# Performance work log

Hardware: AMD Instinct MI355X
Metric: run time of the kernel (lower is better)

The kernel has to match this reference:

```python
import jax, jax.numpy as jnp
import numpy as np

B, S, D = 2, 2048, 1024
N_HEADS = 16
HEAD_DIM = D // N_HEADS  # 64, even for RoPE
THETA = 10000.0


def rope_tables(seq, head_dim, dtype=jnp.float32):
    half = head_dim // 2
    freqs = 1.0 / (THETA ** (jnp.arange(half, dtype=jnp.float32) / half))
    angles = jnp.arange(seq, dtype=jnp.float32)[:, None] * freqs[None, :]  # [S, half]
    return jnp.cos(angles).astype(dtype), jnp.sin(angles).astype(dtype)


def apply_rope_interleaved(x, cos, sin):
    # x: [b, h, s, d]; even/odd interleaving
    x_even = x[..., 0::2]
    x_odd = x[..., 1::2]
    r_even = x_even * cos - x_odd * sin
    r_odd = x_even * sin + x_odd * cos
    # interleave back: stack on last axis then reshape
    out = jnp.stack([r_even, r_odd], axis=-1).reshape(x.shape)
    return out


def setup_inputs() -> dict:
    key = jax.random.key(0)
    ks = jax.random.split(key, 6)
    scale = 1.0 / np.sqrt(D)
    return {
        "x": jax.random.normal(ks[0], (B, S, D), dtype=jnp.float32),
        "Wq": jax.random.normal(ks[1], (D, D), dtype=jnp.float32) * scale,
        "Wk": jax.random.normal(ks[2], (D, D), dtype=jnp.float32) * scale,
        "Wv": jax.random.normal(ks[3], (D, D), dtype=jnp.float32) * scale,
        "Wo": jax.random.normal(ks[4], (D, D), dtype=jnp.float32) * scale,
        "bo": jnp.zeros((D,), dtype=jnp.float32),
    }


def reference(x, Wq, Wk, Wv, Wo, bo):
    b, s, _ = x.shape
    # QKV projections (no bias), split heads -> [b, h, s, hd]
    def proj(W):
        return jnp.einsum('bsd,de->bse', x, W).reshape(b, s, N_HEADS, HEAD_DIM).transpose(0, 2, 1, 3)
    q, k, v = proj(Wq), proj(Wk), proj(Wv)

    cos, sin = rope_tables(s, HEAD_DIM, x.dtype)  # [s, hd//2]
    q = apply_rope_interleaved(q, cos, sin)
    k = apply_rope_interleaved(k, cos, sin)

    scale = 1.0 / jnp.sqrt(jnp.asarray(HEAD_DIM, dtype=x.dtype))
    scores = jnp.einsum('bhqd,bhkd->bhqk', q, k) * scale  # [b, h, s, s]
    causal = jnp.tril(jnp.ones((s, s), dtype=bool))
    scores = jnp.where(causal[None, None], scores, jnp.asarray(-jnp.inf, dtype=scores.dtype))
    attn = jax.nn.softmax(scores, axis=-1)
    ctx = jnp.einsum('bhqk,bhkd->bhqd', attn, v)  # [b, h, s, hd]
    ctx = ctx.transpose(0, 2, 1, 3).reshape(b, s, N_HEADS * HEAD_DIM)
    return jnp.einsum('bsd,de->bse', ctx, Wo) + bo
```

## Files before the change

### kernel.cpp

```cpp
#include <hip/hip_runtime.h>
#include <hip/hip_bf16.h>
#include <math.h>

constexpr int Bb   = 2;
constexpr int S    = 2048;
constexpr int D    = 1024;
constexpr int H    = 16;
constexpr int Dh   = 64;
constexpr int HALF = 32;
constexpr int M    = Bb * S;
constexpr int K    = 1024;
constexpr int N    = 1024;

typedef __attribute__((ext_vector_type(8))) short short8;
typedef __attribute__((ext_vector_type(4))) float f32x4;

__device__ __forceinline__ unsigned short f2bf(float f) {
    unsigned int u = __float_as_uint(f);
    unsigned int r = (u + 0x7fffu + ((u >> 16) & 1u)) >> 16;
    return (unsigned short)r;
}

__device__ __forceinline__ void gl_lds16(const unsigned short* g, unsigned short* lds_base) {
    __builtin_amdgcn_global_load_lds(
        (const __attribute__((address_space(1))) unsigned int*)g,
        (__attribute__((address_space(3))) unsigned int*)lds_base, 16, 0, 0);
}

__global__ __launch_bounds__(256) void prep_kernel(
    const float* __restrict__ x,
    const float* W0, const float* W1, const float* W2, const float* W3,
    unsigned short* __restrict__ xb,
    unsigned short* T0, unsigned short* T1, unsigned short* T2, unsigned short* T3,
    float* __restrict__ cosT, float* __restrict__ sinT)
{
    __shared__ float tile[64][65];
    const int bid = blockIdx.x;
    const int tid = threadIdx.x;

    if (bid < 256) {
        int idx = bid * 256 + tid;
        int s = idx >> 5;
        int i = idx & 31;
        double freq = exp(-(double)i * (log(10000.0) / 32.0));
        double ang  = (double)s * freq;
        cosT[idx] = (float)cos(ang);
        sinT[idx] = (float)sin(ang);
    } else if (bid < 256 + 4096) {
        size_t i = (size_t)(bid - 256) * 256 + tid;
        float4 v = *(const float4*)(x + i * 4);
        ushort4 pk;
        pk.x = f2bf(v.x); pk.y = f2bf(v.y); pk.z = f2bf(v.z); pk.w = f2bf(v.w);
        *(ushort4*)(xb + i * 4) = pk;
    } else {
        int wb = bid - 4352;
        int z  = wb >> 8;
        int rem = wb & 255;
        const float* W = (z == 0) ? W0 : (z == 1) ? W1 : (z == 2) ? W2 : W3;
        unsigned short* T = (z == 0) ? T0 : (z == 1) ? T1 : (z == 2) ? T2 : T3;
        const int bk = (rem >> 4) * 64;
        const int bn = (rem & 15) * 64;
        const int lr = tid >> 4;
        const int lc = (tid & 15) * 4;

        #pragma unroll
        for (int i = 0; i < 4; ++i) {
            int r = lr + i * 16;
            float4 v = *(const float4*)(W + (size_t)(bk + r) * N + bn + lc);
            tile[r][lc + 0] = v.x; tile[r][lc + 1] = v.y;
            tile[r][lc + 2] = v.z; tile[r][lc + 3] = v.w;
        }
        __syncthreads();
        #pragma unroll
        for (int i = 0; i < 4; ++i) {
            int nr = lr + i * 16;
            ushort4 pk;
            pk.x = f2bf(tile[lc + 0][nr]);
            pk.y = f2bf(tile[lc + 1][nr]);
            pk.z = f2bf(tile[lc + 2][nr]);
            pk.w = f2bf(tile[lc + 3][nr]);
            *(ushort4*)(T + (size_t)(bn + nr) * K + bk + lc) = pk;
        }
    }
}

__global__ __launch_bounds__(256) void gemm_qkv_kernel(
    const unsigned short* __restrict__ A,
    const unsigned short* __restrict__ BT,
    unsigned short* outQ, unsigned short* outK, unsigned short* outV,
    const float* __restrict__ cosT, const float* __restrict__ sinT)
{
    constexpr int ABUF = 64 * 32;
    constexpr int BBUF = 128 * 32;
    __shared__ __align__(16) unsigned short As[2 * ABUF];
    __shared__ __align__(16) unsigned short Bs[2 * BBUF];

    const int tid  = threadIdx.x;
    const int wave = tid >> 6;
    const int lane = tid & 63;
    const int col  = lane & 15;
    const int quad = lane >> 4;

    const int mbase = blockIdx.y * 64;
    const int nbase = blockIdx.x * 128;

    const int srow   = lane >> 2;
    const int schunk = lane & 3;

    const unsigned short *pA, *pB0, *pB1;
    {
        int tr = wave * 16 + srow;
        pA  = A + (size_t)(mbase + tr) * K + ((schunk + (tr >> 1)) & 3) * 8;
        int tb0 = wave * 32 + srow;
        int tb1 = wave * 32 + 16 + srow;
        pB0 = BT + (size_t)(nbase + tb0) * K + ((schunk + (tb0 >> 1)) & 3) * 8;
        pB1 = BT + (size_t)(nbase + tb1) * K + ((schunk + (tb1 >> 1)) & 3) * 8;
    }
    unsigned short* dA  = &As[(wave * 16) * 32];
    unsigned short* dB0 = &Bs[(wave * 32) * 32];
    unsigned short* dB1 = &Bs[(wave * 32 + 16) * 32];

    int aoff[4], boff[2];
    #pragma unroll
    for (int mi = 0; mi < 4; ++mi) {
        int r = mi * 16 + col;
        aoff[mi] = r * 32 + ((quad - (r >> 1)) & 3) * 8;
    }
    #pragma unroll
    for (int ni = 0; ni < 2; ++ni) {
        int r = wave * 32 + ni * 16 + col;
        boff[ni] = r * 32 + ((quad - (r >> 1)) & 3) * 8;
    }

    f32x4 acc[4][2];
    #pragma unroll
    for (int mi = 0; mi < 4; ++mi)
        #pragma unroll
        for (int ni = 0; ni < 2; ++ni) acc[mi][ni] = (f32x4)0.f;

    auto stage = [&](int buf) {
        gl_lds16(pA,  dA  + buf * ABUF);  pA  += 32;
        gl_lds16(pB0, dB0 + buf * BBUF);  pB0 += 32;
        gl_lds16(pB1, dB1 + buf * BBUF);  pB1 += 32;
    };
    auto compute = [&](int buf) {
        const unsigned short* Ac = &As[buf * ABUF];
        const unsigned short* Bc = &Bs[buf * BBUF];
        short8 af[4], bfr[2];
        #pragma unroll
        for (int mi = 0; mi < 4; ++mi) af[mi] = *(const short8*)&Ac[aoff[mi]];
        #pragma unroll
        for (int ni = 0; ni < 2; ++ni) bfr[ni] = *(const short8*)&Bc[boff[ni]];
        #pragma unroll
        for (int mi = 0; mi < 4; ++mi)
            #pragma unroll
            for (int ni = 0; ni < 2; ++ni)
                acc[mi][ni] = __builtin_amdgcn_mfma_f32_16x16x32_bf16(af[mi], bfr[ni], acc[mi][ni], 0, 0, 0);
    };

    stage(0);
    #pragma unroll 1
    for (int kk = 0; kk < 32; kk += 2) {
        __syncthreads();
        if (kk + 1 < 32) stage(1);
        compute(0);
        __syncthreads();
        if (kk + 2 < 32) stage(0);
        compute(1);
    }

    const int z = nbase >> 10;
    if (z < 2) {
        unsigned short* o = z ? outK : outQ;
        #pragma unroll
        for (int ni = 0; ni < 2; ++ni) {
            int nl = (nbase & 1023) + wave * 32 + ni * 16 + col;
            int h = nl >> 6, dh0 = nl & 63, p = dh0 >> 1;
            bool even = !(dh0 & 1);
            #pragma unroll
            for (int mi = 0; mi < 4; ++mi)
                #pragma unroll
                for (int reg = 0; reg < 4; ++reg) {
                    int m_g = mbase + mi * 16 + quad * 4 + reg;
                    int b = m_g >> 11, s = m_g & 2047;
                    float v = acc[mi][ni][reg];
                    float part = __shfl_xor(v, 1, 64);
                    float c = cosT[s * HALF + p], sn = sinT[s * HALF + p];
                    float r = even ? (v * c - part * sn) : (v * c + part * sn);
                    o[((size_t)(b * H + h) * S + s) * Dh + dh0] = f2bf(r);
                }
        }
    } else {
        unsigned short* o = outV;
        #pragma unroll
        for (int ni = 0; ni < 2; ++ni) {
            int nl = (nbase & 1023) + wave * 32 + ni * 16 + col;
            int h = nl >> 6, dh0 = nl & 63;
            #pragma unroll
            for (int mi = 0; mi < 4; ++mi) {
                int m0g = mbase + mi * 16 + quad * 4;
                int b = m0g >> 11, s = m0g & 2047;
                ushort4 pk;
                pk.x = f2bf(acc[mi][ni][0]);
                pk.y = f2bf(acc[mi][ni][1]);
                pk.z = f2bf(acc[mi][ni][2]);
                pk.w = f2bf(acc[mi][ni][3]);
                *(ushort4*)&o[((size_t)(b * H + h) * Dh + dh0) * S + s] = pk;
            }
        }
    }
}

__global__ __launch_bounds__(256) void gemm_out_kernel(
    const unsigned short* __restrict__ A,
    const unsigned short* __restrict__ BT,
    float* __restrict__ outO, const float* __restrict__ bias)
{
    constexpr int BK   = 64;
    constexpr int ABUF = 64 * BK;
    constexpr int BBUF = 64 * BK;
    __shared__ __align__(16) unsigned short As[2 * ABUF];
    __shared__ __align__(16) unsigned short Bs[2 * BBUF];

    const int tid  = threadIdx.x;
    const int wave = tid >> 6;
    const int lane = tid & 63;
    const int col  = lane & 15;
    const int quad = lane >> 4;
    const int wy   = wave >> 1;
    const int wx   = wave & 1;

    const int mbase = blockIdx.y * 64;
    const int nbase = blockIdx.x * 64;

    const int srow8 = lane >> 3;
    const int sch8  = lane & 7;

    const unsigned short *pA[2], *pB[2];
    unsigned short *dA[2], *dB[2];
    #pragma unroll
    for (int w = 0; w < 2; ++w) {
        int base = wave * 16 + w * 8;
        int tr = base + srow8;
        pA[w] = A  + (size_t)(mbase + tr) * K + ((sch8 + (tr >> 1)) & 7) * 8;
        pB[w] = BT + (size_t)(nbase + tr) * K + ((sch8 + (tr >> 1)) & 7) * 8;
        dA[w] = &As[base * BK];
        dB[w] = &Bs[base * BK];
    }

    int aoff[2][2], boff[2][2];
    #pragma unroll
    for (int ks = 0; ks < 2; ++ks) {
        #pragma unroll
        for (int mi = 0; mi < 2; ++mi) {
            int r = wy * 32 + mi * 16 + col;
            aoff[ks][mi] = r * BK + (((ks * 4 + quad) - (r >> 1)) & 7) * 8;
        }
        #pragma unroll
        for (int ni = 0; ni < 2; ++ni) {
            int r = wx * 32 + ni * 16 + col;
            boff[ks][ni] = r * BK + (((ks * 4 + quad) - (r >> 1)) & 7) * 8;
        }
    }

    f32x4 acc[2][2];
    #pragma unroll
    for (int mi = 0; mi < 2; ++mi)
        #pragma unroll
        for (int ni = 0; ni < 2; ++ni) acc[mi][ni] = (f32x4)0.f;

    auto stage = [&](int buf) {
        #pragma unroll
        for (int w = 0; w < 2; ++w) { gl_lds16(pA[w], dA[w] + buf * ABUF); pA[w] += BK; }
        #pragma unroll
        for (int w = 0; w < 2; ++w) { gl_lds16(pB[w], dB[w] + buf * BBUF); pB[w] += BK; }
    };
    auto compute = [&](int buf) {
        const unsigned short* Ac = &As[buf * ABUF];
        const unsigned short* Bc = &Bs[buf * BBUF];
        #pragma unroll
        for (int ks = 0; ks < 2; ++ks) {
            short8 af[2], bfr[2];
            #pragma unroll
            for (int mi = 0; mi < 2; ++mi) af[mi] = *(const short8*)&Ac[aoff[ks][mi]];
            #pragma unroll
            for (int ni = 0; ni < 2; ++ni) bfr[ni] = *(const short8*)&Bc[boff[ks][ni]];
            #pragma unroll
            for (int mi = 0; mi < 2; ++mi)
                #pragma unroll
                for (int ni = 0; ni < 2; ++ni)
                    acc[mi][ni] = __builtin_amdgcn_mfma_f32_16x16x32_bf16(af[mi], bfr[ni], acc[mi][ni], 0, 0, 0);
        }
    };

    stage(0);
    #pragma unroll 1
    for (int kk = 0; kk < 16; kk += 2) {
        __syncthreads();
        if (kk + 1 < 16) stage(1);
        compute(0);
        __syncthreads();
        if (kk + 2 < 16) stage(0);
        compute(1);
    }

    #pragma unroll
    for (int ni = 0; ni < 2; ++ni) {
        int n_g = nbase + wx * 32 + ni * 16 + col;
        float bv = bias[n_g];
        #pragma unroll
        for (int mi = 0; mi < 2; ++mi)
            #pragma unroll
            for (int reg = 0; reg < 4; ++reg) {
                int m_g = mbase + wy * 32 + mi * 16 + quad * 4 + reg;
                outO[(size_t)m_g * N + n_g] = acc[mi][ni][reg] + bv;
            }
    }
}

__global__ __launch_bounds__(256) void attn_mfma_kernel(
    const unsigned short* __restrict__ q, const unsigned short* __restrict__ k,
    const unsigned short* __restrict__ vt, unsigned short* __restrict__ ctx)
{
    constexpr int TSZ = 64 * 64;
    __shared__ __align__(16) unsigned short Ks[4 * TSZ];
    __shared__ __align__(16) unsigned short Vs[4 * TSZ];
    __shared__ __align__(16) unsigned short Ps[4][16 * 72];

    const int tid  = threadIdx.x;
    const int wave = tid >> 6;
    const int lane = tid & 63;
    const int col  = lane & 15;
    const int quad = lane >> 4;
    const int l8   = lane >> 3, cp = lane & 7;

    const int bh = blockIdx.y;
    const unsigned short* qb = q  + (size_t)bh * S * Dh;
    const unsigned short* kb = k  + (size_t)bh * S * Dh;
    const unsigned short* vb = vt + (size_t)bh * Dh * S;
    const int b = bh >> 4, h = bh & 15;

    unsigned short* dk0 = &Ks[(wave * 16 + 0) * 64];
    unsigned short* dk1 = &Ks[(wave * 16 + 8) * 64];
    unsigned short* dv0 = &Vs[(wave * 16 + 0) * 64];
    unsigned short* dv1 = &Vs[(wave * 16 + 8) * 64];

    int foff[2][4];
    #pragma unroll
    for (int ks = 0; ks < 2; ++ks)
        #pragma unroll
        for (int nt = 0; nt < 4; ++nt) {
            int r = nt * 16 + col;
            foff[ks][nt] = r * 64 + (((ks * 4 + quad) - r) & 7) * 8;
        }
    int poffW[4][4];
    #pragma unroll
    for (int nt = 0; nt < 4; ++nt)
        #pragma unroll
        for (int reg = 0; reg < 4; ++reg)
            poffW[nt][reg] = (quad * 4 + reg) * 72 + nt * 16 + col;
    const int poffR0 = col * 72 + quad * 8;

    for (int phase = 0; phase < 2; ++phase) {
        const int qt  = phase ? (31 - (int)blockIdx.x) : (int)blockIdx.x;
        const int wr0 = qt * 64 + wave * 16;

        const unsigned short *pk0, *pk1, *pv0, *pv1, *ok0, *ok1, *ov0, *ov1;
        {
            int r0 = wave * 16 + l8, r1 = r0 + 8;
            pk0 = kb + (size_t)r0 * Dh + ((cp + r0) & 7) * 8;
            pk1 = kb + (size_t)r1 * Dh + ((cp + r1) & 7) * 8;
            pv0 = vb + (size_t)r0 * S + ((cp + r0) & 7) * 8;
            pv1 = vb + (size_t)r1 * S + ((cp + r1) & 7) * 8;
            ok0 = pk0 + 64 * Dh; ok1 = pk1 + 64 * Dh;
            ov0 = pv0 + 64;      ov1 = pv1 + 64;
        }

        __syncthreads();
        gl_lds16(pk0, dk0); gl_lds16(pk1, dk1);
        gl_lds16(pv0, dv0); gl_lds16(pv1, dv1);
        if (qt >= 1) {
            gl_lds16(ok0, dk0 + TSZ); gl_lds16(ok1, dk1 + TSZ);
            gl_lds16(ov0, dv0 + TSZ); gl_lds16(ov1, dv1 + TSZ);
        }
        pk0 += 128 * Dh; pk1 += 128 * Dh; pv0 += 128; pv1 += 128;
        ok0 += 128 * Dh; ok1 += 128 * Dh; ov0 += 128; ov1 += 128;

        short8 qfrag[2];
        #pragma unroll
        for (int ks = 0; ks < 2; ++ks)
            qfrag[ks] = *(const short8*)(qb + (size_t)(wr0 + col) * Dh + ks * 32 + quad * 8);

        f32x4 O[4];
        float lacc[4];
        #pragma unroll
        for (int nt = 0; nt < 4; ++nt) O[nt] = (f32x4)0.f;
        #pragma unroll
        for (int r = 0; r < 4; ++r) lacc[r] = 0.f;

        auto subtile = [&](const unsigned short* Kc, const unsigned short* Vc, int t) {
            f32x4 sacc[4];
            #pragma unroll
            for (int nt = 0; nt < 4; ++nt) sacc[nt] = (f32x4)0.f;
            #pragma unroll
            for (int ks = 0; ks < 2; ++ks)
                #pragma unroll
                for (int nt = 0; nt < 4; ++nt) {
                    short8 kf = *(const short8*)&Kc[foff[ks][nt]];
                    sacc[nt] = __builtin_amdgcn_mfma_f32_16x16x32_bf16(qfrag[ks], kf, sacc[nt], 0, 0, 0);
                }
            float pb[4][4];
            #pragma unroll
            for (int nt = 0; nt < 4; ++nt) {
                int key_l = nt * 16 + col;
                #pragma unroll
                for (int reg = 0; reg < 4; ++reg) {
                    float e = __expf(fmaf(sacc[nt][reg], 0.125f, -8.0f));
                    if (t == qt && key_l > wave * 16 + quad * 4 + reg) e = 0.f;
                    pb[nt][reg] = e;
                }
            }
            #pragma unroll
            for (int reg = 0; reg < 4; ++reg)
                lacc[reg] += (pb[0][reg] + pb[1][reg]) + (pb[2][reg] + pb[3][reg]);
            #pragma unroll
            for (int nt = 0; nt < 4; ++nt)
                #pragma unroll
                for (int reg = 0; reg < 4; ++reg)
                    Ps[wave][poffW[nt][reg]] = f2bf(pb[nt][reg]);
            #pragma unroll
            for (int ks = 0; ks < 2; ++ks) {
                short8 pf = *(const short8*)&Ps[wave][poffR0 + ks * 32];
                #pragma unroll
                for (int nt = 0; nt < 4; ++nt) {
                    short8 vf = *(const short8*)&Vc[foff[ks][nt]];
                    O[nt] = __builtin_amdgcn_mfma_f32_16x16x32_bf16(pf, vf, O[nt], 0, 0, 0);
                }
            }
        };

        const int nint = (qt >> 1) + 1;
        for (int i = 0; i < nint; ++i) {
            __syncthreads();
            const int ta = 2 * i;
            if (ta + 2 <= qt) {
                const int nb = ((i + 1) & 1) * 2 * TSZ;
                gl_lds16(pk0, dk0 + nb); gl_lds16(pk1, dk1 + nb);
                gl_lds16(pv0, dv0 + nb); gl_lds16(pv1, dv1 + nb);
                if (ta + 3 <= qt) {
                    gl_lds16(ok0, dk0 + nb + TSZ); gl_lds16(ok1, dk1 + nb + TSZ);
                    gl_lds16(ov0, dv0 + nb + TSZ); gl_lds16(ov1, dv1 + nb + TSZ);
                }
                pk0 += 128 * Dh; pk1 += 128 * Dh; pv0 += 128; pv1 += 128;
                ok0 += 128 * Dh; ok1 += 128 * Dh; ov0 += 128; ov1 += 128;
            }
            const unsigned short* Kc = &Ks[(i & 1) * 2 * TSZ];
            const unsigned short* Vc = &Vs[(i & 1) * 2 * TSZ];
            subtile(Kc, Vc, ta);
            if (ta + 1 <= qt) subtile(Kc + TSZ, Vc + TSZ, ta + 1);
        }

        #pragma unroll
        for (int reg = 0; reg < 4; ++reg) {
            float s = lacc[reg];
            #pragma unroll
            for (int off = 1; off <= 8; off <<= 1)
                s += __shfl_xor(s, off, 64);
            lacc[reg] = s;
        }

        #pragma unroll
        for (int reg = 0; reg < 4; ++reg) {
            float inv = 1.0f / lacc[reg];
            int rg = wr0 + quad * 4 + reg;
            unsigned short* dst = ctx + ((size_t)b * S + rg) * 1024 + h * 64 + col;
            #pragma unroll
            for (int nt = 0; nt < 4; ++nt)
                dst[nt * 16] = f2bf(O[nt][reg] * inv);
        }
    }
}

extern "C" void kernel_launch(void* const* d_in, const int* in_sizes, int n_in,
                              void* d_out, int out_size, void* d_ws, size_t ws_size,
                              hipStream_t stream) {
    const float* x  = (const float*)d_in[0];
    const float* Wq = (const float*)d_in[1];
    const float* Wk = (const float*)d_in[2];
    const float* Wv = (const float*)d_in[3];
    const float* Wo = (const float*)d_in[4];
    const float* bo = (const float*)d_in[5];
    float* out = (float*)d_out;

    const size_t MK  = (size_t)M * K;
    const size_t NK  = (size_t)N * K;
    const size_t QKV = (size_t)Bb * H * S * Dh;

    unsigned short* xb   = (unsigned short*)d_ws;
    unsigned short* WqT  = xb  + MK;
    unsigned short* WkT  = WqT + NK;
    unsigned short* WvT  = WkT + NK;
    unsigned short* WoT  = WvT + NK;
    unsigned short* qbuf = WoT + NK;
    unsigned short* kbuf = qbuf + QKV;
    unsigned short* vtb  = kbuf + QKV;
    unsigned short* ctxb = vtb  + QKV;
    float* cosT = (float*)(ctxb + QKV);
    float* sinT = cosT + (size_t)S * HALF;

    prep_kernel<<<5376, 256, 0, stream>>>(x, Wq, Wk, Wv, Wo,
                                          xb, WqT, WkT, WvT, WoT, cosT, sinT);

    gemm_qkv_kernel<<<dim3(24, 64), 256, 0, stream>>>(
        xb, WqT, qbuf, kbuf, vtb, cosT, sinT);

    attn_mfma_kernel<<<dim3(16, Bb * H), 256, 0, stream>>>(qbuf, kbuf, vtb, ctxb);

    gemm_out_kernel<<<dim3(16, 64), 256, 0, stream>>>(ctxb, WoT, out, bo);
}
```

Measured before the change: 200.2 us.

## Rework QKV GEMM into 256x256 tiles with 4-stage async LDS pipeline

The QKV projection GEMM moves from 64x128 tiles with 4 waves and double buffering to 256x256 tiles with 8 waves. It uses a 4-slot global_load_lds ring with explicit vmcnt/lgkmcnt waits, raw s_barrier and sched_barrier scheduling, and s_setprio around the MFMA bursts. Each K step is split into two halves so A and B prefetches interleave with compute. The aim is more operand reuse per LDS byte and better overlap of global loads with MFMA work. In exchange, the grid drops to 192 blocks, fewer than the CU count, and the kernel uses about 128KB of LDS and many accumulator registers, so occupancy and load balance suffer.

After: 189.2 us. 5.5% less time.

```diff
diff --git a/kernel.cpp b/kernel.cpp
--- a/kernel.cpp
+++ b/kernel.cpp
@@ -84,106 +84,140 @@
     }
 }
 
-__global__ __launch_bounds__(256) void gemm_qkv_kernel(
+__global__ __launch_bounds__(512, 2) void gemm_qkv_kernel(
     const unsigned short* __restrict__ A,
     const unsigned short* __restrict__ BT,
     unsigned short* outQ, unsigned short* outK, unsigned short* outV,
     const float* __restrict__ cosT, const float* __restrict__ sinT)
 {
-    constexpr int ABUF = 64 * 32;
-    constexpr int BBUF = 128 * 32;
-    __shared__ __align__(16) unsigned short As[2 * ABUF];
-    __shared__ __align__(16) unsigned short Bs[2 * BBUF];
+    constexpr int NT   = 32;
+    constexpr int BUFS = 256 * 32;
+    __shared__ __align__(16) unsigned short As[4 * BUFS];
+    __shared__ __align__(16) unsigned short Bs[4 * BUFS];
 
     const int tid  = threadIdx.x;
-    const int wave = tid >> 6;
+    const int wid  = tid >> 6;
     const int lane = tid & 63;
     const int col  = lane & 15;
     const int quad = lane >> 4;
-
-    const int mbase = blockIdx.y * 64;
-    const int nbase = blockIdx.x * 128;
-
-    const int srow   = lane >> 2;
-    const int schunk = lane & 3;
-
-    const unsigned short *pA, *pB0, *pB1;
+    const int wr   = wid >> 2;
+    const int wc   = wid & 3;
+
+    const int mbase = blockIdx.y * 256;
+    const int nbase = blockIdx.x * 256;
+
+    const int srow = lane >> 2;
+    const int sch  = lane & 3;
+    const unsigned short *pA0, *pA1, *pB0, *pB1;
+    unsigned short *dA0, *dA1, *dB0, *dB1;
     {
-        int tr = wave * 16 + srow;
-        pA  = A + (size_t)(mbase + tr) * K + ((schunk + (tr >> 1)) & 3) * 8;
-        int tb0 = wave * 32 + srow;
-        int tb1 = wave * 32 + 16 + srow;
-        pB0 = BT + (size_t)(nbase + tb0) * K + ((schunk + (tb0 >> 1)) & 3) * 8;
-        pB1 = BT + (size_t)(nbase + tb1) * K + ((schunk + (tb1 >> 1)) & 3) * 8;
-    }
-    unsigned short* dA  = &As[(wave * 16) * 32];
-    unsigned short* dB0 = &Bs[(wave * 32) * 32];
-    unsigned short* dB1 = &Bs[(wave * 32 + 16) * 32];
-
-    int aoff[4], boff[2];
-    #pragma unroll
-    for (int mi = 0; mi < 4; ++mi) {
-        int r = mi * 16 + col;
-        aoff[mi] = r * 32 + ((quad - (r >> 1)) & 3) * 8;
-    }
-    #pragma unroll
-    for (int ni = 0; ni < 2; ++ni) {
-        int r = wave * 32 + ni * 16 + col;
-        boff[ni] = r * 32 + ((quad - (r >> 1)) & 3) * 8;
-    }
-
-    f32x4 acc[4][2];
-    #pragma unroll
-    for (int mi = 0; mi < 4; ++mi)
-        #pragma unroll
-        for (int ni = 0; ni < 2; ++ni) acc[mi][ni] = (f32x4)0.f;
-
-    auto stage = [&](int buf) {
-        gl_lds16(pA,  dA  + buf * ABUF);  pA  += 32;
-        gl_lds16(pB0, dB0 + buf * BBUF);  pB0 += 32;
-        gl_lds16(pB1, dB1 + buf * BBUF);  pB1 += 32;
+        int r0 = wid * 16 + srow;
+        int r1 = 128 + wid * 16 + srow;
+        pA0 = A  + (size_t)(mbase + r0) * K + ((sch + (r0 >> 1)) & 3) * 8;
+        pA1 = A  + (size_t)(mbase + r1) * K + ((sch + (r1 >> 1)) & 3) * 8;
+        pB0 = BT + (size_t)(nbase + r0) * K + ((sch + (r0 >> 1)) & 3) * 8;
+        pB1 = BT + (size_t)(nbase + r1) * K + ((sch + (r1 >> 1)) & 3) * 8;
+        dA0 = &As[(wid * 16) * 32];
+        dA1 = &As[(128 + wid * 16) * 32];
+        dB0 = &Bs[(wid * 16) * 32];
+        dB1 = &Bs[(128 + wid * 16) * 32];
+    }
+
+    int aoff[8], boff[4];
+    #pragma unroll
+    for (int f = 0; f < 8; ++f) {
+        int r = wr * 128 + f * 16 + col;
+        aoff[f] = r * 32 + ((quad - (r >> 1)) & 3) * 8;
+    }
+    #pragma unroll
+    for (int n = 0; n < 4; ++n) {
+        int r = wc * 64 + n * 16 + col;
+        boff[n] = r * 32 + ((quad - (r >> 1)) & 3) * 8;
+    }
+
+    f32x4 acc[8][4];
+    #pragma unroll
+    for (int f = 0; f < 8; ++f)
+        #pragma unroll
+        for (int n = 0; n < 4; ++n) acc[f][n] = (f32x4)0.f;
+
+    auto stageA = [&](int slot) {
+        gl_lds16(pA0, dA0 + slot * BUFS); pA0 += 32;
+        gl_lds16(pA1, dA1 + slot * BUFS); pA1 += 32;
     };
-    auto compute = [&](int buf) {
-        const unsigned short* Ac = &As[buf * ABUF];
-        const unsigned short* Bc = &Bs[buf * BBUF];
-        short8 af[4], bfr[2];
-        #pragma unroll
-        for (int mi = 0; mi < 4; ++mi) af[mi] = *(const short8*)&Ac[aoff[mi]];
-        #pragma unroll
-        for (int ni = 0; ni < 2; ++ni) bfr[ni] = *(const short8*)&Bc[boff[ni]];
-        #pragma unroll
-        for (int mi = 0; mi < 4; ++mi)
-            #pragma unroll
-            for (int ni = 0; ni < 2; ++ni)
-                acc[mi][ni] = __builtin_amdgcn_mfma_f32_16x16x32_bf16(af[mi], bfr[ni], acc[mi][ni], 0, 0, 0);
+    auto stageB = [&](int slot) {
+        gl_lds16(pB0, dB0 + slot * BUFS); pB0 += 32;
+        gl_lds16(pB1, dB1 + slot * BUFS); pB1 += 32;
     };
 
-    stage(0);
+    stageA(0); stageB(0);
+    stageA(1); stageB(1);
+    stageA(2); stageB(2);
+    asm volatile("s_waitcnt vmcnt(8)" ::: "memory");
+    __builtin_amdgcn_s_barrier();
+    __builtin_amdgcn_sched_barrier(0);
+
     #pragma unroll 1
-    for (int kk = 0; kk < 32; kk += 2) {
-        __syncthreads();
-        if (kk + 1 < 32) stage(1);
-        compute(0);
-        __syncthreads();
-        if (kk + 2 < 32) stage(0);
-        compute(1);
+    for (int t = 0; t < NT; ++t) {
+        const unsigned short* Ab = &As[(t & 3) * BUFS];
+        const unsigned short* Bc = &Bs[(t & 3) * BUFS];
+        const int nslot = (t + 3) & 3;
+        short8 af[4], bf[4];
+
+        #pragma unroll
+        for (int i = 0; i < 4; ++i) af[i] = *(const short8*)&Ab[aoff[i]];
+        #pragma unroll
+        for (int n = 0; n < 4; ++n) bf[n] = *(const short8*)&Bc[boff[n]];
+        if (t < NT - 3) stageA(nslot);
+        __builtin_amdgcn_sched_barrier(0);
+        __builtin_amdgcn_s_barrier();
+        asm volatile("s_waitcnt lgkmcnt(0)" ::: "memory");
+        __builtin_amdgcn_s_setprio(1);
+        #pragma unroll
+        for (int i = 0; i < 4; ++i)
+            #pragma unroll
+            for (int n = 0; n < 4; ++n)
+                acc[i][n] = __builtin_amdgcn_mfma_f32_16x16x32_bf16(af[i], bf[n], acc[i][n], 0, 0, 0);
+        __builtin_amdgcn_s_setprio(0);
+        __builtin_amdgcn_sched_barrier(0);
+        __builtin_amdgcn_s_barrier();
+        __builtin_amdgcn_sched_barrier(0);
+
+        #pragma unroll
+        for (int i = 0; i < 4; ++i) af[i] = *(const short8*)&Ab[aoff[4 + i]];
+        if (t < NT - 3) stageB(nslot);
+        __builtin_amdgcn_sched_barrier(0);
+        __builtin_amdgcn_s_barrier();
+        asm volatile("s_waitcnt lgkmcnt(0)" ::: "memory");
+        __builtin_amdgcn_s_setprio(1);
+        #pragma unroll
+        for (int i = 0; i < 4; ++i)
+            #pragma unroll
+            for (int n = 0; n < 4; ++n)
+                acc[4 + i][n] = __builtin_amdgcn_mfma_f32_16x16x32_bf16(af[i], bf[n], acc[4 + i][n], 0, 0, 0);
+        __builtin_amdgcn_s_setprio(0);
+        if (t < NT - 3)       { asm volatile("s_waitcnt vmcnt(8)" ::: "memory"); }
+        else if (t == NT - 3) { asm volatile("s_waitcnt vmcnt(4)" ::: "memory"); }
+        else if (t == NT - 2) { asm volatile("s_waitcnt vmcnt(0)" ::: "memory"); }
+        __builtin_amdgcn_s_barrier();
+        __builtin_amdgcn_sched_barrier(0);
     }
 
     const int z = nbase >> 10;
     if (z < 2) {
         unsigned short* o = z ? outK : outQ;
         #pragma unroll
-        for (int ni = 0; ni < 2; ++ni) {
-            int nl = (nbase & 1023) + wave * 32 + ni * 16 + col;
+        for (int n = 0; n < 4; ++n) {
+            int nl = (nbase & 1023) + wc * 64 + n * 16 + col;
             int h = nl >> 6, dh0 = nl & 63, p = dh0 >> 1;
             bool even = !(dh0 & 1);
             #pragma unroll
-            for (int mi = 0; mi < 4; ++mi)
+            for (int f = 0; f < 8; ++f)
                 #pragma unroll
                 for (int reg = 0; reg < 4; ++reg) {
-                    int m_g = mbase + mi * 16 + quad * 4 + reg;
+                    int m_g = mbase + wr * 128 + f * 16 + quad * 4 + reg;
                     int b = m_g >> 11, s = m_g & 2047;
-                    float v = acc[mi][ni][reg];
+                    float v = acc[f][n][reg];
                     float part = __shfl_xor(v, 1, 64);
                     float c = cosT[s * HALF + p], sn = sinT[s * HALF + p];
                     float r = even ? (v * c - part * sn) : (v * c + part * sn);
@@ -191,21 +225,20 @@
                 }
         }
     } else {
-        unsigned short* o = outV;
-        #pragma unroll
-        for (int ni = 0; ni < 2; ++ni) {
-            int nl = (nbase & 1023) + wave * 32 + ni * 16 + col;
+        #pragma unroll
+        for (int n = 0; n < 4; ++n) {
+            int nl = (nbase & 1023) + wc * 64 + n * 16 + col;
             int h = nl >> 6, dh0 = nl & 63;
             #pragma unroll
-            for (int mi = 0; mi < 4; ++mi) {
-                int m0g = mbase + mi * 16 + quad * 4;
-                int b = m0g >> 11, s = m0g & 2047;
+            for (int f = 0; f < 8; ++f) {
+                int m0 = mbase + wr * 128 + f * 16 + quad * 4;
+                int b = m0 >> 11, s = m0 & 2047;
                 ushort4 pk;
-                pk.x = f2bf(acc[mi][ni][0]);
-                pk.y = f2bf(acc[mi][ni][1]);
-                pk.z = f2bf(acc[mi][ni][2]);
-                pk.w = f2bf(acc[mi][ni][3]);
-                *(ushort4*)&o[((size_t)(b * H + h) * Dh + dh0) * S + s] = pk;
+                pk.x = f2bf(acc[f][n][0]);
+                pk.y = f2bf(acc[f][n][1]);
+                pk.z = f2bf(acc[f][n][2]);
+                pk.w = f2bf(acc[f][n][3]);
+                *(ushort4*)&outV[((size_t)(b * H + h) * Dh + dh0) * S + s] = pk;
             }
         }
     }
@@ -511,7 +544,7 @@
     prep_kernel<<<5376, 256, 0, stream>>>(x, Wq, Wk, Wv, Wo,
                                           xb, WqT, WkT, WvT, WoT, cosT, sinT);
 
-    gemm_qkv_kernel<<<dim3(24, 64), 256, 0, stream>>>(
+    gemm_qkv_kernel<<<dim3(12, 16), 512, 0, stream>>>(
         xb, WqT, qbuf, kbuf, vtb, cosT, sinT);
 
     attn_mfma_kernel<<<dim3(16, Bb * H), 256, 0, stream>>>(qbuf, kbuf, vtb, ctxb);
```
